# Optimization experiments

Hardware: AMD Instinct MI355X
Metric: run time of the kernel (lower is better)

Reference implementation:

```python
import jax, jax.numpy as jnp
import numpy as np

SCALE, Z, X, Y = 4, 9, 9, 9
INV_SQRT_2PI = 1.0 / np.sqrt(2.0 * np.pi)


def setup_inputs() -> dict:
    key = jax.random.key(0)
    k1, = jax.random.split(key, 1)
    inp = jax.random.normal(k1, (1, 1, 128, 512, 512), dtype=jnp.float32)
    return {
        "inp": inp,
        "mu_z": jnp.asarray(0.0, dtype=jnp.float32),
        "sig_z": jnp.asarray(0.1, dtype=jnp.float32),
        "bet_xy": jnp.asarray(2.0, dtype=jnp.float32),
        "bet_z": jnp.asarray(1.5, dtype=jnp.float32),
    }


def _gen_alf(bet_xy, bet_z):
    # squared distances along each axis; torch's loop overwrites the wrap-around
    # write, so the net result for odd sizes is simply (arange - size//2)**2
    zd = ((jnp.arange(Z) - Z // 2) ** 2).astype(jnp.float32)[:, None, None]
    xd = ((jnp.arange(X) - X // 2) ** 2).astype(jnp.float32)[None, :, None]
    yd = ((jnp.arange(Y) - Y // 2) ** 2).astype(jnp.float32)[None, None, :]
    d_2 = zd / bet_z ** 2 + (xd + yd) / bet_xy ** 2  # (Z, X, Y)
    return jnp.exp(-d_2 / 2) * INV_SQRT_2PI


def reference(inp, mu_z, sig_z, bet_xy, bet_z):
    z0 = jnp.exp(mu_z + 0.5 * sig_z ** 2)
    rec = inp * z0  # (N, 1, D, H, W)
    alf = _gen_alf(bet_xy, bet_z)[None, None]  # (1, 1, Z, X, Y)
    pad_z = (Z - SCALE + 1) // 2
    rec = jax.lax.conv_general_dilated(
        rec, alf,
        window_strides=(SCALE, 1, 1),
        padding=[(pad_z, pad_z), (X // 2, X // 2), (Y // 2, Y // 2)],
        dimension_numbers=("NCDHW", "OIDHW", "NCDHW"),
    )  # (N, 1, D//SCALE, H, W)
    rec = (rec - rec.min()) / (rec.max() - rec.min())
    return rec
```

## Files before the change

### kernel.cpp

```cpp
#include <hip/hip_runtime.h>

#define D_IN  128
#define D_OUT 32
#define H     512
#define W     512
#define W4    128
#define POS   (H * W4)
#define HB    16
#define ZR    (HB + 8)
#define NTHR  512
#define NPOS  6
#define CONV_GRID ((D_OUT / 2) * (H / HB))

__global__ __launch_bounds__(NTHR)
void conv3d_fused(const float* __restrict__ inp, float* __restrict__ out,
                  const float* __restrict__ bxy_p, const float* __restrict__ bz_p,
                  float* __restrict__ blkMin, float* __restrict__ blkMax) {
    __shared__ float zbuf[ZR * W];
    __shared__ float smin[8], smax[8];

    const int tid = threadIdx.x;
    const int dp = blockIdx.x >> 5;
    const int d  = 2 * dp;
    const int h0 = (blockIdx.x & 31) * HB;

    const float bz = bz_p[0], bx = bxy_p[0];
    const float iz = 1.0f / (2.0f * bz * bz);
    const float ix = 1.0f / (2.0f * bx * bx);
    float wz[9], wx[9];
#pragma unroll
    for (int k = 0; k < 9; ++k) {
        float dd = (float)(k - 4);
        wz[k] = expf(-dd * dd * iz);
        wx[k] = expf(-dd * dd * ix);
    }

    const float4* in4 = (const float4*)inp;
    float4* z4 = (float4*)zbuf;
    const float4 f4z = make_float4(0.f, 0.f, 0.f, 0.f);

    int  rowOff[NPOS];
    bool rowOk[NPOS];
#pragma unroll
    for (int j = 0; j < NPOS; ++j) {
        int pos = j * NTHR + tid;
        int r   = pos >> 7;
        int c4  = pos & (W4 - 1);
        int h   = h0 - 4 + r;
        rowOk[j]  = (unsigned)h < H;
        rowOff[j] = h * W4 + c4;
    }

#define FMA4(A, V, Wc) do { (A).x += (V).x * (Wc); (A).y += (V).y * (Wc); \
                            (A).z += (V).z * (Wc); (A).w += (V).w * (Wc); } while (0)

    const int z0 = 4 * d - 3;
    const bool interior = (dp >= 1) && (dp <= 14);

    float4 accN[NPOS];

#pragma unroll
    for (int j = 0; j < NPOS; ++j) {
        float4 a0 = f4z, a1 = f4z;
        if (rowOk[j]) {
            if (interior) {
                const float4* p = in4 + (size_t)z0 * POS + rowOff[j];
                float4 vv[7];
#pragma unroll
                for (int s = 0; s < 7; ++s) vv[s] = p[s * POS];
                __builtin_amdgcn_sched_barrier(0);
#pragma unroll
                for (int s = 0; s < 7; ++s) FMA4(a0, vv[s], wz[s]);
#pragma unroll
                for (int s = 4; s < 7; ++s) FMA4(a1, vv[s], wz[s - 4]);
                float4 uu[6];
#pragma unroll
                for (int s = 0; s < 6; ++s) uu[s] = p[(s + 7) * POS];
                __builtin_amdgcn_sched_barrier(0);
#pragma unroll
                for (int s = 7; s < 9; ++s)  FMA4(a0, uu[s - 7], wz[s]);
#pragma unroll
                for (int s = 7; s < 13; ++s) FMA4(a1, uu[s - 7], wz[s - 4]);
            } else {
#pragma unroll
                for (int s = 0; s < 13; ++s) {
                    int z = z0 + s;
                    if ((unsigned)z < D_IN) {
                        float4 v = in4[(size_t)z * POS + rowOff[j]];
                        if (s <= 8) FMA4(a0, v, wz[s]);
                        if (s >= 4) FMA4(a1, v, wz[s - 4]);
                    }
                }
            }
        }
        z4[j * NTHR + tid] = a0;
        accN[j] = a1;
    }

    const int lane = tid & 63;
    float lmin =  3.402823466e38f;
    float lmax = -3.402823466e38f;
    float4* out4 = (float4*)out;

    auto hwconv = [&](int dOut) {
        for (int t = tid; t < HB * W4; t += NTHR) {
            int r  = t >> 7;
            int c4 = t & (W4 - 1);

            float4 v = f4z;
#pragma unroll
            for (int k = 0; k < 9; ++k) {
                float4 z = z4[(r + k) * W4 + c4];
                FMA4(v, z, wx[k]);
            }

            float4 va, vc;
            va.x = __shfl_up(v.x, 1, 64);   va.y = __shfl_up(v.y, 1, 64);
            va.z = __shfl_up(v.z, 1, 64);   va.w = __shfl_up(v.w, 1, 64);
            vc.x = __shfl_down(v.x, 1, 64); vc.y = __shfl_down(v.y, 1, 64);
            vc.z = __shfl_down(v.z, 1, 64); vc.w = __shfl_down(v.w, 1, 64);

            if (lane == 0 || lane == 63) {
                int c4n = c4 + ((lane == 0) ? -1 : 1);
                float4 vn = f4z;
                if ((unsigned)c4n < W4) {
#pragma unroll
                    for (int k = 0; k < 9; ++k) {
                        float4 z = z4[(r + k) * W4 + c4n];
                        FMA4(vn, z, wx[k]);
                    }
                }
                if (lane == 0) va = vn; else vc = vn;
            }

            float win[12] = {va.x, va.y, va.z, va.w,
                             v.x,  v.y,  v.z,  v.w,
                             vc.x, vc.y, vc.z, vc.w};
            float4 o = f4z;
#pragma unroll
            for (int k = 0; k < 9; ++k) {
                o.x += win[k]     * wx[k];
                o.y += win[k + 1] * wx[k];
                o.z += win[k + 2] * wx[k];
                o.w += win[k + 3] * wx[k];
            }
            out4[((size_t)dOut * H + h0 + r) * W4 + c4] = o;
            lmin = fminf(lmin, fminf(fminf(o.x, o.y), fminf(o.z, o.w)));
            lmax = fmaxf(lmax, fmaxf(fmaxf(o.x, o.y), fmaxf(o.z, o.w)));
        }
    };

    __syncthreads();
    hwconv(d);
    __syncthreads();
#pragma unroll
    for (int j = 0; j < NPOS; ++j) z4[j * NTHR + tid] = accN[j];
    __syncthreads();
    hwconv(d + 1);

#pragma unroll
    for (int off = 32; off > 0; off >>= 1) {
        lmin = fminf(lmin, __shfl_down(lmin, off, 64));
        lmax = fmaxf(lmax, __shfl_down(lmax, off, 64));
    }
    int wv = tid >> 6;
    if (lane == 0) { smin[wv] = lmin; smax[wv] = lmax; }
    __syncthreads();
    if (tid == 0) {
        float mn = smin[0], mx = smax[0];
#pragma unroll
        for (int i = 1; i < 8; ++i) { mn = fminf(mn, smin[i]); mx = fmaxf(mx, smax[i]); }
        blkMin[blockIdx.x] = mn;
        blkMax[blockIdx.x] = mx;
    }
#undef FMA4
}

#define NORM_NTHR  256
#define NORM_F4_PER_THR 4
#define NORM_GRID  ((D_OUT * H * W4) / (NORM_NTHR * NORM_F4_PER_THR))

__global__ __launch_bounds__(NORM_NTHR)
void norm_kernel(const float* __restrict__ in, float* __restrict__ out,
                 const float* __restrict__ blkMin, const float* __restrict__ blkMax) {
    float lmin =  3.402823466e38f;
    float lmax = -3.402823466e38f;
    for (int i = threadIdx.x; i < CONV_GRID; i += NORM_NTHR) {
        lmin = fminf(lmin, blkMin[i]);
        lmax = fmaxf(lmax, blkMax[i]);
    }
#pragma unroll
    for (int off = 32; off > 0; off >>= 1) {
        lmin = fminf(lmin, __shfl_down(lmin, off, 64));
        lmax = fmaxf(lmax, __shfl_down(lmax, off, 64));
    }
    __shared__ float smin[4], smax[4];
    int lane = threadIdx.x & 63, wv = threadIdx.x >> 6;
    if (lane == 0) { smin[wv] = lmin; smax[wv] = lmax; }
    __syncthreads();
    float mn  = fminf(fminf(smin[0], smin[1]), fminf(smin[2], smin[3]));
    float mx  = fmaxf(fmaxf(smax[0], smax[1]), fmaxf(smax[2], smax[3]));
    float inv = 1.0f / (mx - mn);

    const float4* in4  = (const float4*)in;
    float4*       out4 = (float4*)out;
    int base = blockIdx.x * (NORM_NTHR * NORM_F4_PER_THR) + threadIdx.x;
#pragma unroll
    for (int j = 0; j < NORM_F4_PER_THR; ++j) {
        int idx = base + j * NORM_NTHR;
        float4 v = in4[idx];
        out4[idx] = make_float4((v.x - mn) * inv, (v.y - mn) * inv,
                                (v.z - mn) * inv, (v.w - mn) * inv);
    }
}

extern "C" void kernel_launch(void* const* d_in, const int* in_sizes, int n_in,
                              void* d_out, int out_size, void* d_ws, size_t ws_size,
                              hipStream_t stream) {
    const float* inp    = (const float*)d_in[0];
    const float* bet_xy = (const float*)d_in[3];
    const float* bet_z  = (const float*)d_in[4];
    float* out = (float*)d_out;

    char* ws = (char*)d_ws;
    float* blkMin = (float*)(ws + 4096);
    float* blkMax = (float*)(ws + 8192);
    float* bufA   = (float*)(ws + 65536);

    conv3d_fused<<<CONV_GRID, NTHR, 0, stream>>>(inp, bufA, bet_xy, bet_z, blkMin, blkMax);
    norm_kernel<<<NORM_GRID, NORM_NTHR, 0, stream>>>(bufA, out, blkMin, blkMax);
}
```

Baseline: 240.1 us.

## Compute one output depth slice per block and double-buffer depth loads

Each block now produces a single output depth slice instead of two adjacent ones, which doubles the grid and drops the shared z-overlap reuse between paired slices. The interior depth-load loop is rewritten as a software pipeline with two register buffers, so loads for the next row group are in flight while the current one is reduced. Out-of-range rows are clamped so the loads stay unconditional and are masked afterwards. The cost is more global reads of the overlapping input planes, but the change aims for more parallelism and better latency hiding.

```diff
diff --git a/kernel.cpp b/kernel.cpp
--- a/kernel.cpp
+++ b/kernel.cpp
@@ -10,7 +10,7 @@
 #define ZR    (HB + 8)
 #define NTHR  512
 #define NPOS  6
-#define CONV_GRID ((D_OUT / 2) * (H / HB))
+#define CONV_GRID (D_OUT * (H / HB))
 
 __global__ __launch_bounds__(NTHR)
 void conv3d_fused(const float* __restrict__ inp, float* __restrict__ out,
@@ -20,8 +20,7 @@
     __shared__ float smin[8], smax[8];
 
     const int tid = threadIdx.x;
-    const int dp = blockIdx.x >> 5;
-    const int d  = 2 * dp;
+    const int d  = blockIdx.x >> 5;
     const int h0 = (blockIdx.x & 31) * HB;
 
     const float bz = bz_p[0], bx = bxy_p[0];
@@ -39,7 +38,10 @@
     float4* z4 = (float4*)zbuf;
     const float4 f4z = make_float4(0.f, 0.f, 0.f, 0.f);
 
-    int  rowOff[NPOS];
+#define FMA4(A, V, Wc) do { (A).x += (V).x * (Wc); (A).y += (V).y * (Wc); \
+                            (A).z += (V).z * (Wc); (A).w += (V).w * (Wc); } while (0)
+
+    int  rowOffC[NPOS];
     bool rowOk[NPOS];
 #pragma unroll
     for (int j = 0; j < NPOS; ++j) {
@@ -47,116 +49,108 @@
         int r   = pos >> 7;
         int c4  = pos & (W4 - 1);
         int h   = h0 - 4 + r;
-        rowOk[j]  = (unsigned)h < H;
-        rowOff[j] = h * W4 + c4;
-    }
-
-#define FMA4(A, V, Wc) do { (A).x += (V).x * (Wc); (A).y += (V).y * (Wc); \
-                            (A).z += (V).z * (Wc); (A).w += (V).w * (Wc); } while (0)
-
-    const int z0 = 4 * d - 3;
-    const bool interior = (dp >= 1) && (dp <= 14);
-
-    float4 accN[NPOS];
-
-#pragma unroll
-    for (int j = 0; j < NPOS; ++j) {
-        float4 a0 = f4z, a1 = f4z;
-        if (rowOk[j]) {
-            if (interior) {
-                const float4* p = in4 + (size_t)z0 * POS + rowOff[j];
-                float4 vv[7];
-#pragma unroll
-                for (int s = 0; s < 7; ++s) vv[s] = p[s * POS];
-                __builtin_amdgcn_sched_barrier(0);
-#pragma unroll
-                for (int s = 0; s < 7; ++s) FMA4(a0, vv[s], wz[s]);
-#pragma unroll
-                for (int s = 4; s < 7; ++s) FMA4(a1, vv[s], wz[s - 4]);
-                float4 uu[6];
-#pragma unroll
-                for (int s = 0; s < 6; ++s) uu[s] = p[(s + 7) * POS];
-                __builtin_amdgcn_sched_barrier(0);
-#pragma unroll
-                for (int s = 7; s < 9; ++s)  FMA4(a0, uu[s - 7], wz[s]);
-#pragma unroll
-                for (int s = 7; s < 13; ++s) FMA4(a1, uu[s - 7], wz[s - 4]);
-            } else {
-#pragma unroll
-                for (int s = 0; s < 13; ++s) {
-                    int z = z0 + s;
-                    if ((unsigned)z < D_IN) {
-                        float4 v = in4[(size_t)z * POS + rowOff[j]];
-                        if (s <= 8) FMA4(a0, v, wz[s]);
-                        if (s >= 4) FMA4(a1, v, wz[s - 4]);
-                    }
+        rowOk[j]   = (unsigned)h < H;
+        int hc     = h < 0 ? 0 : (h > H - 1 ? H - 1 : h);
+        rowOffC[j] = hc * W4 + c4;
+    }
+
+    const int dinBase = 4 * d - 3;
+    const bool interior = (d >= 1) && (d <= 30);
+
+    if (interior) {
+        const float4* base = in4 + (ptrdiff_t)dinBase * POS;
+        float4 A[9], B[9];
+
+        auto issue = [&](int j, float4 (&buf)[9]) {
+            const float4* p = base + rowOffC[j];
+#pragma unroll
+            for (int s = 0; s < 9; ++s) buf[s] = p[s * POS];
+        };
+        auto consume = [&](int j, float4 (&buf)[9]) {
+            float4 a0 = f4z;
+#pragma unroll
+            for (int s = 0; s < 9; ++s) FMA4(a0, buf[s], wz[s]);
+            z4[j * NTHR + tid] = rowOk[j] ? a0 : f4z;
+        };
+
+        issue(0, A);
+#pragma unroll
+        for (int j = 0; j < NPOS; ++j) {
+            if (j + 1 < NPOS) {
+                if ((j & 1) == 0) issue(j + 1, B);
+                else              issue(j + 1, A);
+            }
+            __builtin_amdgcn_sched_barrier(0);
+            if ((j & 1) == 0) consume(j, A);
+            else              consume(j, B);
+        }
+    } else {
+#pragma unroll
+        for (int j = 0; j < NPOS; ++j) {
+            float4 a0 = f4z;
+#pragma unroll
+            for (int s = 0; s < 9; ++s) {
+                int z = dinBase + s;
+                if ((unsigned)z < D_IN) {
+                    float4 v = in4[(size_t)z * POS + rowOffC[j]];
+                    FMA4(a0, v, wz[s]);
                 }
             }
-        }
-        z4[j * NTHR + tid] = a0;
-        accN[j] = a1;
-    }
+            z4[j * NTHR + tid] = rowOk[j] ? a0 : f4z;
+        }
+    }
+    __syncthreads();
 
     const int lane = tid & 63;
     float lmin =  3.402823466e38f;
     float lmax = -3.402823466e38f;
     float4* out4 = (float4*)out;
 
-    auto hwconv = [&](int dOut) {
-        for (int t = tid; t < HB * W4; t += NTHR) {
-            int r  = t >> 7;
-            int c4 = t & (W4 - 1);
-
-            float4 v = f4z;
-#pragma unroll
-            for (int k = 0; k < 9; ++k) {
-                float4 z = z4[(r + k) * W4 + c4];
-                FMA4(v, z, wx[k]);
+    for (int t = tid; t < HB * W4; t += NTHR) {
+        int r  = t >> 7;
+        int c4 = t & (W4 - 1);
+
+        float4 v = f4z;
+#pragma unroll
+        for (int k = 0; k < 9; ++k) {
+            float4 z = z4[(r + k) * W4 + c4];
+            FMA4(v, z, wx[k]);
+        }
+
+        float4 va, vc;
+        va.x = __shfl_up(v.x, 1, 64);   va.y = __shfl_up(v.y, 1, 64);
+        va.z = __shfl_up(v.z, 1, 64);   va.w = __shfl_up(v.w, 1, 64);
+        vc.x = __shfl_down(v.x, 1, 64); vc.y = __shfl_down(v.y, 1, 64);
+        vc.z = __shfl_down(v.z, 1, 64); vc.w = __shfl_down(v.w, 1, 64);
+
+        if (lane == 0 || lane == 63) {
+            int c4n = c4 + ((lane == 0) ? -1 : 1);
+            float4 vn = f4z;
+            if ((unsigned)c4n < W4) {
+#pragma unroll
+                for (int k = 0; k < 9; ++k) {
+                    float4 z = z4[(r + k) * W4 + c4n];
+                    FMA4(vn, z, wx[k]);
+                }
             }
-
-            float4 va, vc;
-            va.x = __shfl_up(v.x, 1, 64);   va.y = __shfl_up(v.y, 1, 64);
-            va.z = __shfl_up(v.z, 1, 64);   va.w = __shfl_up(v.w, 1, 64);
-            vc.x = __shfl_down(v.x, 1, 64); vc.y = __shfl_down(v.y, 1, 64);
-            vc.z = __shfl_down(v.z, 1, 64); vc.w = __shfl_down(v.w, 1, 64);
-
-            if (lane == 0 || lane == 63) {
-                int c4n = c4 + ((lane == 0) ? -1 : 1);
-                float4 vn = f4z;
-                if ((unsigned)c4n < W4) {
-#pragma unroll
-                    for (int k = 0; k < 9; ++k) {
-                        float4 z = z4[(r + k) * W4 + c4n];
-                        FMA4(vn, z, wx[k]);
-                    }
-                }
-                if (lane == 0) va = vn; else vc = vn;
-            }
-
-            float win[12] = {va.x, va.y, va.z, va.w,
-                             v.x,  v.y,  v.z,  v.w,
-                             vc.x, vc.y, vc.z, vc.w};
-            float4 o = f4z;
-#pragma unroll
-            for (int k = 0; k < 9; ++k) {
-                o.x += win[k]     * wx[k];
-                o.y += win[k + 1] * wx[k];
-                o.z += win[k + 2] * wx[k];
-                o.w += win[k + 3] * wx[k];
-            }
-            out4[((size_t)dOut * H + h0 + r) * W4 + c4] = o;
-            lmin = fminf(lmin, fminf(fminf(o.x, o.y), fminf(o.z, o.w)));
-            lmax = fmaxf(lmax, fmaxf(fmaxf(o.x, o.y), fmaxf(o.z, o.w)));
-        }
-    };
-
-    __syncthreads();
-    hwconv(d);
-    __syncthreads();
-#pragma unroll
-    for (int j = 0; j < NPOS; ++j) z4[j * NTHR + tid] = accN[j];
-    __syncthreads();
-    hwconv(d + 1);
+            if (lane == 0) va = vn; else vc = vn;
+        }
+
+        float win[12] = {va.x, va.y, va.z, va.w,
+                         v.x,  v.y,  v.z,  v.w,
+                         vc.x, vc.y, vc.z, vc.w};
+        float4 o = f4z;
+#pragma unroll
+        for (int k = 0; k < 9; ++k) {
+            o.x += win[k]     * wx[k];
+            o.y += win[k + 1] * wx[k];
+            o.z += win[k + 2] * wx[k];
+            o.w += win[k + 3] * wx[k];
+        }
+        out4[((size_t)d * H + h0 + r) * W4 + c4] = o;
+        lmin = fminf(lmin, fminf(fminf(o.x, o.y), fminf(o.z, o.w)));
+        lmax = fmaxf(lmax, fmaxf(fmaxf(o.x, o.y), fmaxf(o.z, o.w)));
+    }
 
 #pragma unroll
     for (int off = 32; off > 0; off >>= 1) {
```

Result: slower. 252.2 us (+5.1%).
